# Kernel optimization log

Hardware: AMD Instinct MI355X
Metric: run time of the kernel (lower is better)

## Reference

```python
import jax, jax.numpy as jnp
import numpy as np

D_MODEL = 1024
N_HEADS = 16
D_HEAD = D_MODEL // N_HEADS
B, T = 4, 2048


def setup_inputs() -> dict:
    key = jax.random.key(0)
    ks = jax.random.split(key, 5)
    scale = 1.0 / np.sqrt(D_MODEL)
    return {
        "x": jax.random.normal(ks[0], (B, T, D_MODEL), dtype=jnp.float32),
        "W_Q": jax.random.normal(ks[1], (D_MODEL, D_MODEL), dtype=jnp.float32) * scale,
        "W_K": jax.random.normal(ks[2], (D_MODEL, D_MODEL), dtype=jnp.float32) * scale,
        "W_V": jax.random.normal(ks[3], (D_MODEL, D_MODEL), dtype=jnp.float32) * scale,
        "W_O": jax.random.normal(ks[4], (D_MODEL, D_MODEL), dtype=jnp.float32) * scale,
    }


def reference(x, W_Q, W_K, W_V, W_O):
    b, t, c = x.shape
    # nn.Linear applies x @ W.T; weights stored [out, in]
    def heads(w):
        return (x @ w.T).reshape(b, t, N_HEADS, D_HEAD).transpose(0, 2, 1, 3)  # b h t d
    q, k, v = heads(W_Q), heads(W_K), heads(W_V)
    scores = jnp.einsum("bhqd,bhkd->bhqk", q, k) / jnp.sqrt(jnp.float32(D_HEAD))
    causal = jnp.tril(jnp.ones((t, t), dtype=bool))
    scores = jnp.where(causal, scores, -jnp.inf)
    attn = jax.nn.softmax(scores, axis=-1)
    out = jnp.einsum("bhqk,bhkd->bhqd", attn, v)
    out = out.transpose(0, 2, 1, 3).reshape(b, t, c)
    return out @ W_O.T
```

## Files before the change

kernel.cpp:

```cpp
#include <hip/hip_runtime.h>
#include <stdint.h>
#include <stddef.h>

#define SEQ 2048
#define NH 16
#define DH 64
#define DM 1024
#define NROWS 8192

typedef __attribute__((ext_vector_type(4))) float f32x4;
typedef __attribute__((ext_vector_type(16))) float f32x16;
typedef __attribute__((ext_vector_type(8))) short s16x8;
typedef __attribute__((ext_vector_type(4))) unsigned u32x4;

__device__ __forceinline__ unsigned short f2bf(float f) {
  unsigned int u = __builtin_bit_cast(unsigned int, f);
  u += 0x7fffu + ((u >> 16) & 1u);
  return (unsigned short)(u >> 16);
}

__device__ __forceinline__ float exp2fast(float x) {
#if __has_builtin(__builtin_amdgcn_exp2f)
  return __builtin_amdgcn_exp2f(x);
#else
  return exp2f(x);
#endif
}

__device__ __forceinline__ float rcpfast(float x) {
#if __has_builtin(__builtin_amdgcn_rcpf)
  return __builtin_amdgcn_rcpf(x);
#else
  return 1.0f / x;
#endif
}

__device__ __forceinline__ unsigned pk2(float lo, float hi) {
  return __builtin_amdgcn_perm(__builtin_bit_cast(unsigned, hi),
                               __builtin_bit_cast(unsigned, lo), 0x07060302u);
}


__device__ __forceinline__ void async16(const void* g, void* l) {
  __builtin_amdgcn_global_load_lds(
      (const __attribute__((address_space(1))) unsigned int*)g,
      (__attribute__((address_space(3))) unsigned int*)l, 16, 0, 0);
}

__global__ __launch_bounds__(256) void cast_all(const float* __restrict__ x,
                                                const float* __restrict__ w0,
                                                const float* __restrict__ w1,
                                                const float* __restrict__ w2,
                                                const float* __restrict__ w3,
                                                short* __restrict__ Xb,
                                                short* __restrict__ Wb) {
  int g = blockIdx.x * 256 + threadIdx.x;
  const float* src;
  short* dst;
  int off;
  if (g < NROWS * DM / 8) {
    src = x; dst = Xb; off = g;
  } else {
    int r = g - NROWS * DM / 8;
    int w = r >> 17;
    off = r & 131071;
    src = (w == 0) ? w0 : (w == 1) ? w1 : (w == 2) ? w2 : w3;
    dst = Wb + ((size_t)w << 20);
  }
  const float4* s4 = (const float4*)src;
  float4 a = s4[2 * off], b = s4[2 * off + 1];
  s16x8 o;
  o[0] = (short)f2bf(a.x); o[1] = (short)f2bf(a.y);
  o[2] = (short)f2bf(a.z); o[3] = (short)f2bf(a.w);
  o[4] = (short)f2bf(b.x); o[5] = (short)f2bf(b.y);
  o[6] = (short)f2bf(b.z); o[7] = (short)f2bf(b.w);
  *(s16x8*)(dst + (size_t)8 * off) = o;
}

__global__ __launch_bounds__(256, 2) void gemm_qkv(const short* __restrict__ X,
                                                   const short* __restrict__ Wq,
                                                   const short* __restrict__ Wk,
                                                   const short* __restrict__ Wv,
                                                   short* __restrict__ Qo,
                                                   short* __restrict__ Ko,
                                                   short* __restrict__ Vo) {
  __shared__ __align__(16) short Xs[128 * 64];
  __shared__ __align__(16) short Ws[3][128 * 64];
  const int tid = threadIdx.x;
  const int lane = tid & 63, wave = tid >> 6;
  const int l15 = lane & 15, quad = lane >> 4;
  const int bn = blockIdx.x * 128;
  const int bm = blockIdx.y * 128;
  const int wm = (wave >> 1) * 64, wn = (wave & 1) * 64;

  const short* Ab = X + (size_t)bm * DM;
  const short* W0 = Wq + (size_t)bn * DM;
  const short* W1 = Wk + (size_t)bn * DM;
  const short* W2 = Wv + (size_t)bn * DM;

  f32x4 acc[3][4][4];
#pragma unroll
  for (int g = 0; g < 3; g++)
#pragma unroll
    for (int i = 0; i < 4; i++)
#pragma unroll
      for (int j = 0; j < 4; j++) acc[g][i][j] = (f32x4)0.f;

  for (int k0 = 0; k0 < DM; k0 += 64) {
#pragma unroll
    for (int i = 0; i < 4; i++) {
      int f = i * 256 + tid;
      int row = f >> 3, c = ((f & 7) ^ (row & 7)) * 8;
      async16(Ab + (size_t)row * DM + k0 + c, Xs + (size_t)f * 8);
      async16(W0 + (size_t)row * DM + k0 + c, &Ws[0][(size_t)f * 8]);
      async16(W1 + (size_t)row * DM + k0 + c, &Ws[1][(size_t)f * 8]);
      async16(W2 + (size_t)row * DM + k0 + c, &Ws[2][(size_t)f * 8]);
    }
    __syncthreads();
#pragma unroll
    for (int ks = 0; ks < 2; ks++) {
      s16x8 af[4];
#pragma unroll
      for (int t = 0; t < 4; t++)
        af[t] = *(const s16x8*)(Xs + (wm + t * 16 + l15) * 64 + (((ks * 4 + quad) ^ (l15 & 7)) * 8));
#pragma unroll
      for (int g = 0; g < 3; g++) {
        s16x8 bfr[4];
#pragma unroll
        for (int t = 0; t < 4; t++)
          bfr[t] = *(const s16x8*)(&Ws[g][(wn + t * 16 + l15) * 64 + (((ks * 4 + quad) ^ (l15 & 7)) * 8)]);
#pragma unroll
        for (int mt = 0; mt < 4; mt++)
#pragma unroll
          for (int nt = 0; nt < 4; nt++) {
            if (g == 2)
              acc[2][mt][nt] = __builtin_amdgcn_mfma_f32_16x16x32_bf16(bfr[nt], af[mt], acc[2][mt][nt], 0, 0, 0);
            else
              acc[g][mt][nt] = __builtin_amdgcn_mfma_f32_16x16x32_bf16(af[mt], bfr[nt], acc[g][mt][nt], 0, 0, 0);
          }
      }
    }
    __syncthreads();
  }

#pragma unroll
  for (int g = 0; g < 2; g++) {
    short* Dst = g ? Ko : Qo;
#pragma unroll
    for (int mt = 0; mt < 4; mt++)
#pragma unroll
      for (int r = 0; r < 4; r++)
#pragma unroll
        for (int nt = 0; nt < 4; nt++) {
          int m = bm + wm + mt * 16 + quad * 4 + r;
          int n = bn + wn + nt * 16 + l15;
          int b = m >> 11, t = m & (SEQ - 1);
          int hh = n >> 6, d = n & 63;
          Dst[((((size_t)b * NH + hh) * SEQ + t) << 6) + d] = (short)f2bf(acc[g][mt][nt][r]);
        }
  }
#pragma unroll
  for (int mt = 0; mt < 4; mt++)
#pragma unroll
    for (int r = 0; r < 4; r++)
#pragma unroll
      for (int nt = 0; nt < 4; nt++) {
        int n = bn + wn + nt * 16 + quad * 4 + r;
        int m = bm + wm + mt * 16 + l15;
        int b = m >> 11, t = m & (SEQ - 1);
        int hh = n >> 6, d = n & 63;
        Vo[(((size_t)b * NH + hh) * DH + d) * SEQ + t] = (short)f2bf(acc[2][mt][nt][r]);
      }
}

__global__ __launch_bounds__(256, 2) void gemm_o(const short* __restrict__ A,
                                                 const short* __restrict__ B,
                                                 float* __restrict__ C) {
  __shared__ __align__(16) short As[256 * 64];
  __shared__ __align__(16) short Bs[128 * 64];
  const int tid = threadIdx.x;
  const int lane = tid & 63, wave = tid >> 6;
  const int l15 = lane & 15, quad = lane >> 4;
  const int bm = blockIdx.y * 256, bn = blockIdx.x * 128;
  const int wm = (wave >> 1) * 128, wn = (wave & 1) * 64;

  const short* Ab = A + (size_t)bm * DM;
  const short* Bb = B + (size_t)bn * DM;

  f32x4 acc[8][4];
#pragma unroll
  for (int i = 0; i < 8; i++)
#pragma unroll
    for (int j = 0; j < 4; j++) acc[i][j] = (f32x4)0.f;

  for (int k0 = 0; k0 < DM; k0 += 64) {
#pragma unroll
    for (int i = 0; i < 8; i++) {
      int f = i * 256 + tid;
      int row = f >> 3, c = ((f & 7) ^ (row & 7)) * 8;
      async16(Ab + (size_t)row * DM + k0 + c, As + (size_t)f * 8);
    }
#pragma unroll
    for (int i = 0; i < 4; i++) {
      int f = i * 256 + tid;
      int row = f >> 3, c = ((f & 7) ^ (row & 7)) * 8;
      async16(Bb + (size_t)row * DM + k0 + c, Bs + (size_t)f * 8);
    }
    __syncthreads();
#pragma unroll
    for (int ks = 0; ks < 2; ks++) {
      s16x8 bfr[4];
#pragma unroll
      for (int t = 0; t < 4; t++)
        bfr[t] = *(const s16x8*)(Bs + (wn + t * 16 + l15) * 64 + (((ks * 4 + quad) ^ (l15 & 7)) * 8));
#pragma unroll
      for (int mt = 0; mt < 8; mt++) {
        s16x8 af = *(const s16x8*)(As + (wm + mt * 16 + l15) * 64 + (((ks * 4 + quad) ^ (l15 & 7)) * 8));
#pragma unroll
        for (int nt = 0; nt < 4; nt++)
          acc[mt][nt] = __builtin_amdgcn_mfma_f32_16x16x32_bf16(af, bfr[nt], acc[mt][nt], 0, 0, 0);
      }
    }
    __syncthreads();
  }

#pragma unroll
  for (int mt = 0; mt < 8; mt++)
#pragma unroll
    for (int r = 0; r < 4; r++) {
      int m = bm + wm + mt * 16 + quad * 4 + r;
#pragma unroll
      for (int nt = 0; nt < 4; nt++)
        C[(size_t)m * DM + bn + wn + nt * 16 + l15] = acc[mt][nt][r];
    }
}

__global__ __launch_bounds__(256, 2) void attn_kernel(const short* __restrict__ Q,
                                                      const short* __restrict__ K,
                                                      const short* __restrict__ V,
                                                      short* __restrict__ O) {
  __shared__ __align__(16) short Smem[2 * 16384];

  const int tid = threadIdx.x;
  const int lane = tid & 63, wave = tid >> 6;
  const int l31 = lane & 31, h = lane >> 5;

  const int r = blockIdx.x & 63;
  const int qt = 15 - (blockIdx.x >> 6);
  const int bh = (r & 7) * 8 + (r >> 3);
  const int q0 = qt * 128;

  const short* Qb = Q + (size_t)bh * SEQ * DH;
  const short* Kb = K + (size_t)bh * SEQ * DH;
  const short* Vb = V + (size_t)bh * DH * SEQ;

  auto stageK = [&](int ktile, int buf) {
    short* base = Smem + buf * 16384;
    const short* ksrc = Kb + (size_t)ktile * 128 * DH;
#pragma unroll
    for (int i = 0; i < 4; i++) {
      int f = i * 256 + tid;
      int kk = f >> 3, c8 = (f & 7) ^ (kk & 7);
      async16(ksrc + (size_t)kk * DH + c8 * 8, base + (size_t)f * 8);
    }
  };
  auto stageV = [&](int ktile, int buf) {
    short* base = Smem + buf * 16384 + 8192;
    const short* vsrc = Vb + (size_t)ktile * 128;
#pragma unroll
    for (int i = 0; i < 4; i++) {
      int f = i * 256 + tid;
      int d = f >> 4, c16 = (f & 15) ^ (d & 15);
      async16(vsrc + (size_t)d * SEQ + c16 * 8, base + (size_t)f * 8);
    }
  };

  s16x8 qf[4];
#pragma unroll
  for (int ks = 0; ks < 4; ks++)
    qf[ks] = *(const s16x8*)(Qb + (size_t)(q0 + wave * 32 + l31) * DH + ks * 16 + h * 8);

  f32x16 oacc[2];
  oacc[0] = (f32x16)0.f;
  oacc[1] = (f32x16)0.f;
  float m_own = -3.0e38f, l_own = 0.f, aprev = 0.f;
  s16x8 pf[8];
  const float C = 0.18033688011112042f;

  stageK(0, 0);

  for (int kt = 0; kt <= qt; kt++) {
    const int cur = kt & 1;
    __syncthreads();
    if (kt < qt) stageK(kt + 1, cur ^ 1);
    stageV(kt, cur);
    const short* Ks = Smem + cur * 16384;

    f32x16 sacc[4];
#pragma unroll
    for (int T = 0; T < 4; T++) sacc[T] = (f32x16)0.f;
#pragma unroll
    for (int ks = 0; ks < 4; ks++) {
#pragma unroll
      for (int T = 0; T < 4; T++) {
        s16x8 kf = *(const s16x8*)(Ks + (T * 32 + l31) * 64 + (((2 * ks + h) ^ (l31 & 7)) * 8));
        sacc[T] = __builtin_amdgcn_mfma_f32_32x32x16_bf16(kf, qf[ks], sacc[T], 0, 0, 0);
      }
    }

    if (kt > 0) {
      const short* Vp = Smem + (cur ^ 1) * 16384 + 8192;
#pragma unroll
      for (int r2 = 0; r2 < 16; r2++) {
        oacc[0][r2] *= aprev;
        oacc[1][r2] *= aprev;
      }
#pragma unroll
      for (int kc = 0; kc < 8; kc++) {
#pragma unroll
        for (int td = 0; td < 2; td++) {
          s16x8 vf = *(const s16x8*)(Vp + (td * 32 + l31) * 128 + (((2 * kc + h) ^ (l31 & 15)) * 8));
          oacc[td] = __builtin_amdgcn_mfma_f32_32x32x16_bf16(vf, pf[kc], oacc[td], 0, 0, 0);
        }
      }
    }

    if (kt == qt) {
      int limit = wave * 32 + l31 - 4 * h;
#pragma unroll
      for (int T = 0; T < 4; T++)
#pragma unroll
        for (int r2 = 0; r2 < 16; r2++) {
          int kkc = T * 32 + (r2 & 3) + 8 * (r2 >> 2);
          if (kkc > limit) sacc[T][r2] = -3.0e38f;
        }
    }

    float tm[4];
#pragma unroll
    for (int T = 0; T < 4; T++) {
      float a = fmaxf(fmaxf(sacc[T][0], sacc[T][1]), fmaxf(sacc[T][2], sacc[T][3]));
      float b = fmaxf(fmaxf(sacc[T][4], sacc[T][5]), fmaxf(sacc[T][6], sacc[T][7]));
      float cc = fmaxf(fmaxf(sacc[T][8], sacc[T][9]), fmaxf(sacc[T][10], sacc[T][11]));
      float d = fmaxf(fmaxf(sacc[T][12], sacc[T][13]), fmaxf(sacc[T][14], sacc[T][15]));
      tm[T] = fmaxf(fmaxf(a, b), fmaxf(cc, d));
    }
    float mx = fmaxf(fmaxf(tm[0], tm[1]), fmaxf(tm[2], tm[3]));
    mx = fmaxf(mx, __shfl_xor(mx, 32, 64));
    float mnew = fmaxf(m_own, mx);
    float mb = mnew * C;
    float alpha = exp2fast(m_own * C - mb);
    m_own = mnew;

    float ts[4];
#pragma unroll
    for (int T = 0; T < 4; T++) {
#pragma unroll
      for (int r2 = 0; r2 < 16; r2++) sacc[T][r2] = exp2fast(fmaf(sacc[T][r2], C, -mb));
      float a = (sacc[T][0] + sacc[T][1]) + (sacc[T][2] + sacc[T][3]);
      float b = (sacc[T][4] + sacc[T][5]) + (sacc[T][6] + sacc[T][7]);
      float cc = (sacc[T][8] + sacc[T][9]) + (sacc[T][10] + sacc[T][11]);
      float d = (sacc[T][12] + sacc[T][13]) + (sacc[T][14] + sacc[T][15]);
      ts[T] = (a + b) + (cc + d);
    }
    float rsum = (ts[0] + ts[1]) + (ts[2] + ts[3]);
    rsum += __shfl_xor(rsum, 32, 64);
    l_own = l_own * alpha + rsum;

#pragma unroll
    for (int T = 0; T < 4; T++) {
      unsigned P0 = pk2(sacc[T][0], sacc[T][1]);
      unsigned P1 = pk2(sacc[T][2], sacc[T][3]);
      unsigned P2 = pk2(sacc[T][4], sacc[T][5]);
      unsigned P3 = pk2(sacc[T][6], sacc[T][7]);
      unsigned P4 = pk2(sacc[T][8], sacc[T][9]);
      unsigned P5 = pk2(sacc[T][10], sacc[T][11]);
      unsigned P6 = pk2(sacc[T][12], sacc[T][13]);
      unsigned P7 = pk2(sacc[T][14], sacc[T][15]);
      unsigned R0 = (unsigned)__shfl_xor((int)(h ? P0 : P2), 32, 64);
      unsigned R1 = (unsigned)__shfl_xor((int)(h ? P1 : P3), 32, 64);
      unsigned R2 = (unsigned)__shfl_xor((int)(h ? P4 : P6), 32, 64);
      unsigned R3 = (unsigned)__shfl_xor((int)(h ? P5 : P7), 32, 64);
      u32x4 lo, hi;
      lo[0] = h ? R0 : P0; lo[1] = h ? R1 : P1; lo[2] = h ? P2 : R0; lo[3] = h ? P3 : R1;
      hi[0] = h ? R2 : P4; hi[1] = h ? R3 : P5; hi[2] = h ? P6 : R2; hi[3] = h ? P7 : R3;
      pf[2 * T] = __builtin_bit_cast(s16x8, lo);
      pf[2 * T + 1] = __builtin_bit_cast(s16x8, hi);
    }

    aprev = alpha;
  }

  __syncthreads();
  {
    const short* Vp = Smem + (qt & 1) * 16384 + 8192;
#pragma unroll
    for (int r2 = 0; r2 < 16; r2++) {
      oacc[0][r2] *= aprev;
      oacc[1][r2] *= aprev;
    }
#pragma unroll
    for (int kc = 0; kc < 8; kc++) {
#pragma unroll
      for (int td = 0; td < 2; td++) {
        s16x8 vf = *(const s16x8*)(Vp + (td * 32 + l31) * 128 + (((2 * kc + h) ^ (l31 & 15)) * 8));
        oacc[td] = __builtin_amdgcn_mfma_f32_32x32x16_bf16(vf, pf[kc], oacc[td], 0, 0, 0);
      }
    }
  }
  __syncthreads();

  const int b = bh >> 4, head = bh & 15;
  float inv = rcpfast(l_own);
  const int g = lane >> 3, d4 = (lane & 7) * 4;
#pragma unroll
  for (int td = 0; td < 2; td++) {
    float* tb = (float*)Smem + (size_t)(wave * 2 + td) * 1056;
#pragma unroll
    for (int r2 = 0; r2 < 16; r2++) {
      int d_loc = (r2 & 3) + 8 * (r2 >> 2) + 4 * h;
      tb[d_loc * 33 + l31] = oacc[td][r2] * inv;
    }
#pragma unroll
    for (int j = 0; j < 4; j++) {
      int qq = j * 8 + g;
      float x0 = tb[(d4 + 0) * 33 + qq];
      float x1 = tb[(d4 + 1) * 33 + qq];
      float x2 = tb[(d4 + 2) * 33 + qq];
      float x3 = tb[(d4 + 3) * 33 + qq];
      uint2 pkd;
      pkd.x = (unsigned)f2bf(x0) | ((unsigned)f2bf(x1) << 16);
      pkd.y = (unsigned)f2bf(x2) | ((unsigned)f2bf(x3) << 16);
      int q = q0 + wave * 32 + qq;
      *(uint2*)(O + ((size_t)(b * SEQ + q)) * DM + head * DH + td * 32 + d4) = pkd;
    }
  }
}

extern "C" void kernel_launch(void* const* d_in, const int* in_sizes, int n_in,
                              void* d_out, int out_size, void* d_ws, size_t ws_size,
                              hipStream_t stream) {
  const float* x  = (const float*)d_in[0];
  const float* wq = (const float*)d_in[1];
  const float* wk = (const float*)d_in[2];
  const float* wv = (const float*)d_in[3];
  const float* wo = (const float*)d_in[4];

  short* ws = (short*)d_ws;
  short* Xb  = ws;
  short* Wqb = Xb + (size_t)NROWS * DM;
  short* Wkb = Wqb + (size_t)DM * DM;
  short* Wvb = Wkb + (size_t)DM * DM;
  short* Wob = Wvb + (size_t)DM * DM;
  short* Qb  = Wob + (size_t)DM * DM;
  short* Kb  = Qb + (size_t)NROWS * DM;
  short* Vtb = Kb + (size_t)NROWS * DM;
  short* Ob  = Xb;

  int total_chunks = NROWS * DM / 8 + 4 * (DM * DM / 8);
  cast_all<<<total_chunks / 256, 256, 0, stream>>>(x, wq, wk, wv, wo, Xb, Wqb);

  gemm_qkv<<<dim3(8, 64), 256, 0, stream>>>(Xb, Wqb, Wkb, Wvb, Qb, Kb, Vtb);

  attn_kernel<<<1024, 256, 0, stream>>>(Qb, Kb, Vtb, Ob);

  gemm_o<<<dim3(8, 32), 256, 0, stream>>>(Ob, Wob, (float*)d_out);
}
```

Before: 253.7 us.

## Double-buffer QKV GEMM with 256-row tiles, 8 waves and BK=32

The QKV projection GEMM now uses 512 threads per block on a 256x128 tile. K-steps of 32 are staged into two dynamic shared-memory buffers, so the async loads of the next K-slice overlap the MFMAs on the current one. The XOR swizzle is redone for 32-wide rows. Bigger M tiles reuse each weight tile across more rows and halve the grid. The cost is 80 KB of LDS and more waves per block, which may limit occupancy.

```diff
diff --git a/kernel.cpp b/kernel.cpp
--- a/kernel.cpp
+++ b/kernel.cpp
@@ -77,20 +77,19 @@
   *(s16x8*)(dst + (size_t)8 * off) = o;
 }
 
-__global__ __launch_bounds__(256, 2) void gemm_qkv(const short* __restrict__ X,
+__global__ __launch_bounds__(512, 2) void gemm_qkv(const short* __restrict__ X,
                                                    const short* __restrict__ Wq,
                                                    const short* __restrict__ Wk,
                                                    const short* __restrict__ Wv,
                                                    short* __restrict__ Qo,
                                                    short* __restrict__ Ko,
                                                    short* __restrict__ Vo) {
-  __shared__ __align__(16) short Xs[128 * 64];
-  __shared__ __align__(16) short Ws[3][128 * 64];
+  extern __shared__ __align__(16) short smem[];
   const int tid = threadIdx.x;
   const int lane = tid & 63, wave = tid >> 6;
   const int l15 = lane & 15, quad = lane >> 4;
   const int bn = blockIdx.x * 128;
-  const int bm = blockIdx.y * 128;
+  const int bm = blockIdx.y * 256;
   const int wm = (wave >> 1) * 64, wn = (wave & 1) * 64;
 
   const short* Ab = X + (size_t)bm * DM;
@@ -106,39 +105,56 @@
 #pragma unroll
       for (int j = 0; j < 4; j++) acc[g][i][j] = (f32x4)0.f;
 
-  for (int k0 = 0; k0 < DM; k0 += 64) {
-#pragma unroll
-    for (int i = 0; i < 4; i++) {
-      int f = i * 256 + tid;
-      int row = f >> 3, c = ((f & 7) ^ (row & 7)) * 8;
-      async16(Ab + (size_t)row * DM + k0 + c, Xs + (size_t)f * 8);
-      async16(W0 + (size_t)row * DM + k0 + c, &Ws[0][(size_t)f * 8]);
-      async16(W1 + (size_t)row * DM + k0 + c, &Ws[1][(size_t)f * 8]);
-      async16(W2 + (size_t)row * DM + k0 + c, &Ws[2][(size_t)f * 8]);
-    }
-    __syncthreads();
-#pragma unroll
-    for (int ks = 0; ks < 2; ks++) {
-      s16x8 af[4];
+  auto stage = [&](int k, int buf) {
+    short* base = smem + buf * 20480;
+    const int k0 = k * 32;
+#pragma unroll
+    for (int i = 0; i < 2; i++) {
+      int f = i * 512 + tid;
+      int row = f >> 2;
+      int c = ((f & 3) ^ (row & 3) ^ ((row >> 2) & 1)) * 8;
+      async16(Ab + (size_t)row * DM + k0 + c, base + (size_t)f * 8);
+    }
+    {
+      int f = tid;
+      int row = f >> 2;
+      int c = ((f & 3) ^ (row & 3) ^ ((row >> 2) & 1)) * 8;
+      size_t go = (size_t)row * DM + k0 + c;
+      async16(W0 + go, base + 8192 + (size_t)f * 8);
+      async16(W1 + go, base + 12288 + (size_t)f * 8);
+      async16(W2 + go, base + 16384 + (size_t)f * 8);
+    }
+  };
+
+  stage(0, 0);
+  __syncthreads();
+
+  const int sl = (l15 & 3) ^ ((l15 >> 2) & 1);
+  for (int k = 0; k < 32; k++) {
+    const int buf = k & 1;
+    if (k < 31) stage(k + 1, buf ^ 1);
+    const short* base = smem + buf * 20480;
+
+    s16x8 af[4];
+#pragma unroll
+    for (int t = 0; t < 4; t++)
+      af[t] = *(const s16x8*)(base + (size_t)(wm + t * 16 + l15) * 32 + (size_t)((quad ^ sl) * 8));
+#pragma unroll
+    for (int g = 0; g < 3; g++) {
+      const short* wb = base + 8192 + g * 4096;
+      s16x8 bfr[4];
 #pragma unroll
       for (int t = 0; t < 4; t++)
-        af[t] = *(const s16x8*)(Xs + (wm + t * 16 + l15) * 64 + (((ks * 4 + quad) ^ (l15 & 7)) * 8));
-#pragma unroll
-      for (int g = 0; g < 3; g++) {
-        s16x8 bfr[4];
-#pragma unroll
-        for (int t = 0; t < 4; t++)
-          bfr[t] = *(const s16x8*)(&Ws[g][(wn + t * 16 + l15) * 64 + (((ks * 4 + quad) ^ (l15 & 7)) * 8)]);
-#pragma unroll
-        for (int mt = 0; mt < 4; mt++)
-#pragma unroll
-          for (int nt = 0; nt < 4; nt++) {
-            if (g == 2)
-              acc[2][mt][nt] = __builtin_amdgcn_mfma_f32_16x16x32_bf16(bfr[nt], af[mt], acc[2][mt][nt], 0, 0, 0);
-            else
-              acc[g][mt][nt] = __builtin_amdgcn_mfma_f32_16x16x32_bf16(af[mt], bfr[nt], acc[g][mt][nt], 0, 0, 0);
-          }
-      }
+        bfr[t] = *(const s16x8*)(wb + (size_t)(wn + t * 16 + l15) * 32 + (size_t)((quad ^ sl) * 8));
+#pragma unroll
+      for (int mt = 0; mt < 4; mt++)
+#pragma unroll
+        for (int nt = 0; nt < 4; nt++) {
+          if (g == 2)
+            acc[2][mt][nt] = __builtin_amdgcn_mfma_f32_16x16x32_bf16(bfr[nt], af[mt], acc[2][mt][nt], 0, 0, 0);
+          else
+            acc[g][mt][nt] = __builtin_amdgcn_mfma_f32_16x16x32_bf16(af[mt], bfr[nt], acc[g][mt][nt], 0, 0, 0);
+        }
     }
     __syncthreads();
   }
@@ -457,10 +473,17 @@
   short* Vtb = Kb + (size_t)NROWS * DM;
   short* Ob  = Xb;
 
+  static bool attr_done = false;
+  if (!attr_done) {
+    (void)hipFuncSetAttribute((const void*)gemm_qkv,
+                              hipFuncAttributeMaxDynamicSharedMemorySize, 81920);
+    attr_done = true;
+  }
+
   int total_chunks = NROWS * DM / 8 + 4 * (DM * DM / 8);
   cast_all<<<total_chunks / 256, 256, 0, stream>>>(x, wq, wk, wv, wo, Xb, Wqb);
 
-  gemm_qkv<<<dim3(8, 64), 256, 0, stream>>>(Xb, Wqb, Wkb, Wvb, Qb, Kb, Vtb);
+  gemm_qkv<<<dim3(8, 32), 512, 81920, stream>>>(Xb, Wqb, Wkb, Wvb, Qb, Kb, Vtb);
 
   attn_kernel<<<1024, 256, 0, stream>>>(Qb, Kb, Vtb, Ob);
 
```

Measured after the change: 245.1 us. 3.4% less time.
